# Kernel optimization log

Measured on AMD Instinct MI355X. Metric: run time of the kernel, lower is better.

The kernel has to match this reference:

```python
import jax, jax.numpy as jnp
import numpy as np

DIM = 1024
DIM_HEAD = 64
HEADS = 16
BATCH = 2
SEQ = 2048
SCALE = DIM_HEAD ** -0.5


def setup_inputs() -> dict:
    key = jax.random.key(0)
    ks = jax.random.split(key, 5)
    tokens = jax.random.normal(ks[0], (BATCH, SEQ, DIM), dtype=jnp.float32)
    wq = jax.random.normal(ks[1], (HEADS, DIM, DIM_HEAD), dtype=jnp.float32)
    wk = jax.random.normal(ks[2], (HEADS, DIM, DIM_HEAD), dtype=jnp.float32)
    wv = jax.random.normal(ks[3], (HEADS, DIM, DIM_HEAD), dtype=jnp.float32)
    wo = jax.random.normal(ks[4], (HEADS, DIM_HEAD, DIM), dtype=jnp.float32)
    return {"tokens": tokens, "wq": wq, "wk": wk, "wv": wv, "wo": wo}


def reference(tokens, wq, wk, wv, wo):
    # q, k, v: [b, h, n, dh]
    q = jnp.einsum('bnd,hde->bhne', tokens, wq) * SCALE
    k = jnp.einsum('bnd,hde->bhne', tokens, wk)
    v = jnp.einsum('bnd,hde->bhne', tokens, wv)
    sim = jnp.einsum('bhie,bhje->bhij', q, k)          # [b, h, n, n]
    attn = jax.nn.softmax(sim, axis=-1)
    aggregated = jnp.einsum('bhij,bhje->bhie', attn, v)  # [b, h, n, dh]
    retrieved = jnp.einsum('bhne,hed->bnd', aggregated, wo)  # sum over heads
    return retrieved
```

## Files before the change

kernel.cpp:

```cpp
#include <hip/hip_runtime.h>
#include <hip/hip_fp16.h>
#include <stdint.h>

#define BB 2
#define HH 16
#define SS 2048
#define DD 1024
#define DHH 64
#define QSCALE 0.18033688011112042f

typedef _Float16 half8 __attribute__((ext_vector_type(8)));
typedef _Float16 half4 __attribute__((ext_vector_type(4)));
typedef __fp16 fp16x2 __attribute__((ext_vector_type(2)));
typedef float floatx4 __attribute__((ext_vector_type(4)));

__device__ __forceinline__ floatx4 mfma16(half8 a, half8 b, floatx4 c) {
  return __builtin_amdgcn_mfma_f32_16x16x32_f16(a, b, c, 0, 0, 0);
}
__device__ __forceinline__ floatx4 mfma16k16(half4 a, half4 b, floatx4 c) {
  return __builtin_amdgcn_mfma_f32_16x16x16f16(a, b, c, 0, 0, 0);
}

__device__ __forceinline__ void dma16(const _Float16* g, _Float16* l) {
  __builtin_amdgcn_global_load_lds(
      (const __attribute__((address_space(1))) uint32_t*)g,
      (__attribute__((address_space(3))) uint32_t*)l,
      16, 0, 0);
}

__global__ __launch_bounds__(256) void convert_kernel(
    const float* __restrict__ wq, const float* __restrict__ wk,
    const float* __restrict__ wv, const float* __restrict__ wo,
    _Float16* __restrict__ Wh, _Float16* __restrict__ Wl,
    _Float16* __restrict__ Wot)
{
  __shared__ float St[64][68];
  const int kt = blockIdx.x;
  const int hy = blockIdx.y;
  const int z  = blockIdx.z;
  const int t  = (int)threadIdx.x;
  const int k0 = kt * 64;

  const float* src = (z == 0) ? (wq + hy * (DD * DHH))
                   : (z == 1) ? (wk + hy * (DD * DHH))
                   : (z == 2) ? (wv + hy * (DD * DHH))
                   : wo;

  const int rr = t >> 4, cc = (t & 15) * 4;
  if (z < 3) {
    #pragma unroll
    for (int i = 0; i < 4; ++i)
      *(floatx4*)&St[rr + 16 * i][cc] =
          *(const floatx4*)(src + (k0 + rr + 16 * i) * DHH + cc);
  } else {
    const int d0 = hy * 64;
    #pragma unroll
    for (int i = 0; i < 4; ++i)
      *(floatx4*)&St[rr + 16 * i][cc] =
          *(const floatx4*)(src + (k0 + rr + 16 * i) * 1024 + d0 + cc);
  }
  __syncthreads();

  const int e = t >> 2, kc = (t & 3) * 16;
  if (z < 3) {
    const int n = z * 1024 + hy * 64 + e;
    half8 hi0, hi1, lo0, lo1;
    #pragma unroll
    for (int u = 0; u < 16; ++u) {
      float x = St[kc + u][e];
      _Float16 hh = (_Float16)x;
      _Float16 ll = (_Float16)(x - (float)hh);
      if (u < 8) { hi0[u] = hh; lo0[u] = ll; }
      else       { hi1[u - 8] = hh; lo1[u - 8] = ll; }
    }
    *(half8*)(Wh + n * 1024 + k0 + kc)     = hi0;
    *(half8*)(Wh + n * 1024 + k0 + kc + 8) = hi1;
    *(half8*)(Wl + n * 1024 + k0 + kc)     = lo0;
    *(half8*)(Wl + n * 1024 + k0 + kc + 8) = lo1;
  } else {
    const int d0 = hy * 64;
    half8 hi0, hi1;
    #pragma unroll
    for (int u = 0; u < 16; ++u) {
      _Float16 hh = (_Float16)St[kc + u][e];
      if (u < 8) hi0[u] = hh; else hi1[u - 8] = hh;
    }
    *(half8*)(Wot + (d0 + e) * 1024 + k0 + kc)     = hi0;
    *(half8*)(Wot + (d0 + e) * 1024 + k0 + kc + 8) = hi1;
  }
}

__global__ __launch_bounds__(256) void tokens_split_kernel(
    const float* __restrict__ tokens,
    _Float16* __restrict__ th, _Float16* __restrict__ tl)
{
  const int i = ((int)blockIdx.x * 256 + (int)threadIdx.x) * 8;
  floatx4 x0 = *(const floatx4*)(tokens + i);
  floatx4 x1 = *(const floatx4*)(tokens + i + 4);
  half8 h, l;
  #pragma unroll
  for (int j = 0; j < 8; ++j) {
    float x = (j < 4) ? x0[j] : x1[j - 4];
    _Float16 hh = (_Float16)x;
    h[j] = hh;
    l[j] = (_Float16)(x - (float)hh);
  }
  *(half8*)(th + i) = h;
  *(half8*)(tl + i) = l;
}

__global__ __launch_bounds__(512) void qkv_gemm_kernel(
    const _Float16* __restrict__ th, const _Float16* __restrict__ tl,
    const _Float16* __restrict__ Wh, const _Float16* __restrict__ Wl,
    _Float16* __restrict__ qh, _Float16* __restrict__ ql,
    _Float16* __restrict__ kh, _Float16* __restrict__ kl,
    _Float16* __restrict__ vt)
{
  __shared__ alignas(16) _Float16 sbuf[4][4][128 * 32];

  const int n0 = blockIdx.x * 128;
  const int m0 = blockIdx.y * 128;
  const int zb = n0 >> 10;
  const bool is_v = (zb == 2);
  const int t = (int)threadIdx.x;
  const int lane = t & 63, wid = t >> 6;
  const int l16 = lane & 15, q4 = lane >> 4;
  const int mw = (wid & 3) * 32, nw = (wid >> 2) * 64;

  const int g  = (lane & 7) ^ ((lane >> 3) & 7);
  const int grow  = (lane >> 3) * 2 + (g >> 2);
  const int gcol8 = (g & 3) * 8;
  const int laneoff = (l16 >> 1) * 128 + (((((l16 & 1) << 2) | q4) ^ (l16 >> 1)) * 16);

  const int arr = wid & 3;
  const int rowb = (wid >> 2) * 64;
  const _Float16* src = (arr == 0) ? (th + m0 * 1024)
                      : (arr == 1) ? (Wh + n0 * 1024)
                      : (arr == 2) ? (Wl + n0 * 1024)
                      :              (tl + m0 * 1024);
  const bool stage_active = !(is_v && arr == 3);
  const _Float16* gsrc = src + (rowb + grow) * 1024 + gcol8;

  const floatx4 z4 = {0.0f, 0.0f, 0.0f, 0.0f};
  floatx4 acc[2][4];
  #pragma unroll
  for (int mi = 0; mi < 2; ++mi)
    #pragma unroll
    for (int ni = 0; ni < 4; ++ni) acc[mi][ni] = z4;

  auto stage = [&](int buf, int kt2) {
    if (stage_active) {
      const _Float16* gp = gsrc + kt2 * 32;
      _Float16* dst = &sbuf[buf][arr][rowb * 32];
      #pragma unroll
      for (int j = 0; j < 4; ++j)
        dma16(gp + j * 16 * 1024, dst + j * 16 * 32);
    }
  };

  auto compute = [&](int buf) {
    const char* sAh = (const char*)&sbuf[buf][0][0];
    const char* sBh = (const char*)&sbuf[buf][1][0];
    const char* sBl = (const char*)&sbuf[buf][2][0];
    const char* sAl = (const char*)&sbuf[buf][3][0];
    half8 a_h[2], b_h[4], b_l[4];
    #pragma unroll
    for (int mi = 0; mi < 2; ++mi)
      a_h[mi] = *(const half8*)(sAh + (mw + mi * 16) * 64 + laneoff);
    #pragma unroll
    for (int ni = 0; ni < 4; ++ni) {
      b_h[ni] = *(const half8*)(sBh + (nw + ni * 16) * 64 + laneoff);
      b_l[ni] = *(const half8*)(sBl + (nw + ni * 16) * 64 + laneoff);
    }
    #pragma unroll
    for (int ni = 0; ni < 4; ++ni)
      #pragma unroll
      for (int mi = 0; mi < 2; ++mi)
        acc[mi][ni] = mfma16(a_h[mi], b_h[ni], acc[mi][ni]);
    if (!is_v) {
      half8 a_l[2];
      #pragma unroll
      for (int mi = 0; mi < 2; ++mi)
        a_l[mi] = *(const half8*)(sAl + (mw + mi * 16) * 64 + laneoff);
      #pragma unroll
      for (int ni = 0; ni < 4; ++ni)
        #pragma unroll
        for (int mi = 0; mi < 2; ++mi)
          acc[mi][ni] = mfma16(a_l[mi], b_h[ni], acc[mi][ni]);
    }
    #pragma unroll
    for (int ni = 0; ni < 4; ++ni)
      #pragma unroll
      for (int mi = 0; mi < 2; ++mi)
        acc[mi][ni] = mfma16(a_h[mi], b_l[ni], acc[mi][ni]);
  };

  stage(0, 0);
  stage(1, 1);
  stage(2, 2);

#define QKV_PHASE(P, BUF, VC)                                  \
  asm volatile("s_waitcnt vmcnt(" #VC ")" ::: "memory");       \
  __builtin_amdgcn_s_barrier();                                \
  if ((P) + 3 < 32) stage(((P) + 3) & 3, (P) + 3);             \
  compute(BUF);

  #pragma unroll 1
  for (int p4 = 0; p4 < 28; p4 += 4) {
    QKV_PHASE(p4 + 0, 0, 8)
    QKV_PHASE(p4 + 1, 1, 8)
    QKV_PHASE(p4 + 2, 2, 8)
    QKV_PHASE(p4 + 3, 3, 8)
  }
  QKV_PHASE(28, 0, 8)
  QKV_PHASE(29, 1, 8)
  QKV_PHASE(30, 2, 4)
  QKV_PHASE(31, 3, 0)
#undef QKV_PHASE

  #pragma unroll
  for (int ni = 0; ni < 4; ++ni) {
    const int ncol = n0 + nw + ni * 16;
    const int h = (ncol >> 6) & 15;
    const int e = (ncol & 63) + l16;
    #pragma unroll
    for (int mi = 0; mi < 2; ++mi) {
      #pragma unroll
      for (int r = 0; r < 4; ++r) {
        const int grow2 = m0 + mw + mi * 16 + q4 * 4 + r;
        const int b = grow2 >> 11, s = grow2 & 2047;
        const float v = acc[mi][ni][r];
        const int qkidx = ((b * HH + h) * SS + s) * DHH + e;
        if (zb == 0) {
          const float vs = v * QSCALE;
          const _Float16 hh = (_Float16)vs;
          qh[qkidx] = hh;
          ql[qkidx] = (_Float16)(vs - (float)hh);
        } else if (zb == 1) {
          const _Float16 hh = (_Float16)v;
          kh[qkidx] = hh;
          kl[qkidx] = (_Float16)(v - (float)hh);
        } else {
          const int sl = s & 63;
          const int sp = (s & ~63) | ((sl & 48) >> 2) | ((sl & 12) << 2) | (sl & 3);
          vt[((b * HH + h) * DHH + e) * SS + sp] = (_Float16)v;
        }
      }
    }
  }
}

__global__ __launch_bounds__(512) void attn_kernel(
    const _Float16* __restrict__ qh, const _Float16* __restrict__ ql,
    const _Float16* __restrict__ kh, const _Float16* __restrict__ kl,
    const _Float16* __restrict__ vt, _Float16* __restrict__ agg)
{
  __shared__ _Float16 Kh[2][64][72], Kl[2][64][72];
  __shared__ _Float16 Vs[2][64][64];

  const int qt = blockIdx.x;
  const int h  = blockIdx.y;
  const int b  = blockIdx.z;
  const int bh = b * HH + h;
  const int t = (int)threadIdx.x;
  const int lane = t & 63, wid = t >> 6;
  const int l16 = lane & 15, q4 = lane >> 4;

  const int sr = t >> 3, sc = (t & 7) * 8;
  const int vsw = ((t & 7) ^ (sr & 7)) * 8;

  const int vch0 = ((2 * q4 + 0) ^ (l16 & 7)) * 8;
  const int vch1 = ((2 * q4 + 1) ^ (l16 & 7)) * 8;

  half8 qfh[2], qfl[2];
  {
    const int s = qt * 128 + wid * 16 + l16;
    const int base = (bh * SS + s) * DHH + q4 * 8;
    qfh[0] = *(const half8*)(qh + base);
    qfh[1] = *(const half8*)(qh + base + 32);
    qfl[0] = *(const half8*)(ql + base);
    qfl[1] = *(const half8*)(ql + base + 32);
  }

  const floatx4 z4 = {0.0f, 0.0f, 0.0f, 0.0f};
  floatx4 o[4];
  #pragma unroll
  for (int i = 0; i < 4; ++i) o[i] = z4;
  float m_r = -1e30f;
  float l_lane = 0.0f;

  half8 pK, pL, pV;
  {
    const int gk = (bh * SS + sr) * DHH + sc;
    pK = *(const half8*)(kh + gk);
    pL = *(const half8*)(kl + gk);
    pV = *(const half8*)(vt + (bh * DHH + sr) * SS + sc);
  }
  *(half8*)&Kh[0][sr][sc] = pK;
  *(half8*)&Kl[0][sr][sc] = pL;
  *(half8*)&Vs[0][sr][vsw] = pV;
  __syncthreads();
  {
    const int gk = (bh * SS + 64 + sr) * DHH + sc;
    pK = *(const half8*)(kh + gk);
    pL = *(const half8*)(kl + gk);
    pV = *(const half8*)(vt + (bh * DHH + sr) * SS + 64 + sc);
  }

  auto body = [&](int buf, int kt) {
    floatx4 sv[4];
    __builtin_amdgcn_s_setprio(1);
    #pragma unroll
    for (int sub = 0; sub < 4; ++sub) {
      const half8 ah0 = *(const half8*)&Kh[buf][sub * 16 + l16][q4 * 8];
      const half8 ah1 = *(const half8*)&Kh[buf][sub * 16 + l16][q4 * 8 + 32];
      const half8 al0 = *(const half8*)&Kl[buf][sub * 16 + l16][q4 * 8];
      const half8 al1 = *(const half8*)&Kl[buf][sub * 16 + l16][q4 * 8 + 32];
      floatx4 s4 = z4;
      s4 = mfma16(ah0, qfh[0], s4);
      s4 = mfma16(ah1, qfh[1], s4);
      s4 = mfma16(al0, qfh[0], s4);
      s4 = mfma16(al1, qfh[1], s4);
      s4 = mfma16(ah0, qfl[0], s4);
      s4 = mfma16(ah1, qfl[1], s4);
      sv[sub] = s4;
    }
    __builtin_amdgcn_s_setprio(0);

    float m0 = fmaxf(fmaxf(sv[0][0], sv[0][1]), fmaxf(sv[0][2], sv[0][3]));
    float m1 = fmaxf(fmaxf(sv[1][0], sv[1][1]), fmaxf(sv[1][2], sv[1][3]));
    float m2 = fmaxf(fmaxf(sv[2][0], sv[2][1]), fmaxf(sv[2][2], sv[2][3]));
    float m3 = fmaxf(fmaxf(sv[3][0], sv[3][1]), fmaxf(sv[3][2], sv[3][3]));
    const float mx = fmaxf(fmaxf(m0, m1), fmaxf(m2, m3));

    if (__any(mx > m_r + 8.0f)) {
      float mc = fmaxf(mx, __shfl_xor(mx, 16));
      mc = fmaxf(mc, __shfl_xor(mc, 32));
      const float mnew = fmaxf(m_r, mc);
      const float alpha = exp2f(m_r - mnew);
      m_r = mnew;
      l_lane *= alpha;
      #pragma unroll
      for (int sub = 0; sub < 4; ++sub)
        #pragma unroll
        for (int r = 0; r < 4; ++r) o[sub][r] *= alpha;
    }

    half4 p4[4];
    #pragma unroll
    for (int c = 0; c < 4; ++c) {
      const float p0 = exp2f(sv[c][0] - m_r);
      const float p1 = exp2f(sv[c][1] - m_r);
      const float p2 = exp2f(sv[c][2] - m_r);
      const float p3 = exp2f(sv[c][3] - m_r);
      l_lane += (p0 + p1) + (p2 + p3);
      const fp16x2 a01 = __builtin_amdgcn_cvt_pkrtz(p0, p1);
      const fp16x2 a23 = __builtin_amdgcn_cvt_pkrtz(p2, p3);
      half4 pv;
      pv[0] = (_Float16)a01[0]; pv[1] = (_Float16)a01[1];
      pv[2] = (_Float16)a23[0]; pv[3] = (_Float16)a23[1];
      p4[c] = pv;
    }

    if (kt < 31) {
      *(half8*)&Kh[buf ^ 1][sr][sc] = pK;
      *(half8*)&Kl[buf ^ 1][sr][sc] = pL;
      *(half8*)&Vs[buf ^ 1][sr][vsw] = pV;
    }

    __builtin_amdgcn_s_setprio(1);
    #pragma unroll
    for (int sub = 0; sub < 4; ++sub) {
      const half8 v01 = *(const half8*)&Vs[buf][sub * 16 + l16][vch0];
      const half8 v23 = *(const half8*)&Vs[buf][sub * 16 + l16][vch1];
      const half4 va0 = {v01[0], v01[1], v01[2], v01[3]};
      const half4 va1 = {v01[4], v01[5], v01[6], v01[7]};
      const half4 va2 = {v23[0], v23[1], v23[2], v23[3]};
      const half4 va3 = {v23[4], v23[5], v23[6], v23[7]};
      o[sub] = mfma16k16(va0, p4[0], o[sub]);
      o[sub] = mfma16k16(va1, p4[1], o[sub]);
      o[sub] = mfma16k16(va2, p4[2], o[sub]);
      o[sub] = mfma16k16(va3, p4[3], o[sub]);
    }
    __builtin_amdgcn_s_setprio(0);

    __syncthreads();

    if (kt < 30) {
      const int k2 = (kt + 2) * 64;
      const int gk = (bh * SS + k2 + sr) * DHH + sc;
      pK = *(const half8*)(kh + gk);
      pL = *(const half8*)(kl + gk);
      pV = *(const half8*)(vt + (bh * DHH + sr) * SS + k2 + sc);
    }
  };

  #pragma unroll 1
  for (int kt = 0; kt < 32; kt += 2) {
    body(0, kt);
    body(1, kt + 1);
  }

  float lsum = l_lane;
  lsum += __shfl_xor(lsum, 16);
  lsum += __shfl_xor(lsum, 32);
  const float inv = 1.0f / lsum;
  const int s = qt * 128 + wid * 16 + l16;
  #pragma unroll
  for (int sub = 0; sub < 4; ++sub) {
    half4 ov;
    #pragma unroll
    for (int r = 0; r < 4; ++r) ov[r] = (_Float16)(o[sub][r] * inv);
    *(half4*)(agg + (b * SS + s) * (HH * DHH) + h * DHH + sub * 16 + q4 * 4) = ov;
  }
}

__global__ __launch_bounds__(256) void out_gemm_kernel(
    const _Float16* __restrict__ agg, const _Float16* __restrict__ Wot,
    float* __restrict__ out)
{
  __shared__ alignas(16) _Float16 sbuf[2][2][128 * 32];
  const int n0 = blockIdx.x * 128;
  const int m0 = blockIdx.y * 128;
  const int t = (int)threadIdx.x;
  const int lane = t & 63, wid = t >> 6;
  const int l16 = lane & 15, q4 = lane >> 4;
  const int mw = (wid & 1) * 64, nw = (wid >> 1) * 64;

  const int g  = (lane & 7) ^ ((lane >> 3) & 7);
  const int grow  = (lane >> 3) * 2 + (g >> 2);
  const int gcol8 = (g & 3) * 8;
  const int laneoff = (l16 >> 1) * 128 + (((((l16 & 1) << 2) | q4) ^ (l16 >> 1)) * 16);

  const int arr = wid >> 1;
  const int half64 = (wid & 1) * 64;
  const _Float16* src = (arr == 0) ? (agg + m0 * 1024) : (Wot + n0 * 1024);
  const _Float16* gsrc = src + (half64 + grow) * 1024 + gcol8;

  const floatx4 z4 = {0.0f, 0.0f, 0.0f, 0.0f};
  floatx4 acc[4][4];
  #pragma unroll
  for (int mi = 0; mi < 4; ++mi)
    #pragma unroll
    for (int ni = 0; ni < 4; ++ni) acc[mi][ni] = z4;

  auto stage = [&](int buf, int kt2) {
    const _Float16* gp = gsrc + kt2 * 32;
    _Float16* dst = &sbuf[buf][arr][half64 * 32];
    #pragma unroll
    for (int j = 0; j < 4; ++j)
      dma16(gp + j * 16 * 1024, dst + j * 16 * 32);
  };

  auto compute = [&](int buf) {
    const char* sA = (const char*)&sbuf[buf][0][0];
    const char* sB = (const char*)&sbuf[buf][1][0];
    half8 a_f[4];
    #pragma unroll
    for (int mi = 0; mi < 4; ++mi)
      a_f[mi] = *(const half8*)(sA + (mw + mi * 16) * 64 + laneoff);
    #pragma unroll
    for (int ni = 0; ni < 4; ++ni) {
      const half8 b_f = *(const half8*)(sB + (nw + ni * 16) * 64 + laneoff);
      #pragma unroll
      for (int mi = 0; mi < 4; ++mi)
        acc[mi][ni] = mfma16(a_f[mi], b_f, acc[mi][ni]);
    }
  };

  stage(0, 0);
  __syncthreads();

  #pragma unroll 1
  for (int kt = 0; kt < 32; kt += 2) {
    if (kt + 1 < 32) stage(1, kt + 1);
    compute(0);
    __syncthreads();
    if (kt + 2 < 32) stage(0, kt + 2);
    compute(1);
    __syncthreads();
  }

  #pragma unroll
  for (int ni = 0; ni < 4; ++ni)
    #pragma unroll
    for (int mi = 0; mi < 4; ++mi)
      #pragma unroll
      for (int r = 0; r < 4; ++r)
        out[(m0 + mw + mi * 16 + q4 * 4 + r) * 1024 + n0 + nw + ni * 16 + l16] =
            acc[mi][ni][r];
}

extern "C" void kernel_launch(void* const* d_in, const int* in_sizes, int n_in,
                              void* d_out, int out_size, void* d_ws, size_t ws_size,
                              hipStream_t stream)
{
  const float* tokens = (const float*)d_in[0];
  const float* wq = (const float*)d_in[1];
  const float* wk = (const float*)d_in[2];
  const float* wv = (const float*)d_in[3];
  const float* wo = (const float*)d_in[4];
  float* out = (float*)d_out;

  char* ws = (char*)d_ws;
  _Float16* qh  = (_Float16*)(ws);
  _Float16* ql  = (_Float16*)(ws + 8388608);
  _Float16* kh  = (_Float16*)(ws + 16777216);
  _Float16* kl  = (_Float16*)(ws + 25165824);
  _Float16* vt  = (_Float16*)(ws + 33554432);
  _Float16* Wh  = (_Float16*)(ws + 41943040);
  _Float16* Wl  = (_Float16*)(ws + 48234496);
  _Float16* Wot = (_Float16*)(ws + 54525952);
  _Float16* th  = (_Float16*)(ws + 56623104);
  _Float16* tl  = (_Float16*)(ws + 65011712);
  _Float16* agg = (_Float16*)(ws + 56623104);

  convert_kernel<<<dim3(16, 16, 4), 256, 0, stream>>>(wq, wk, wv, wo, Wh, Wl, Wot);
  tokens_split_kernel<<<2048, 256, 0, stream>>>(tokens, th, tl);
  qkv_gemm_kernel<<<dim3(24, 32), 512, 0, stream>>>(th, tl, Wh, Wl, qh, ql, kh, kl, vt);
  attn_kernel<<<dim3(16, 16, 2), 512, 0, stream>>>(qh, ql, kh, kl, vt, agg);
  out_gemm_kernel<<<dim3(8, 32), 256, 0, stream>>>(agg, Wot, out);
}
```

Before: 287.5 us.

## Load V fragments straight into registers, use fast exp2, deepen out-GEMM pipeline

The attention kernel now loads V tiles directly from global memory into per-lane register fragments, double-buffered across iterations, instead of staging them through shared memory. This removes the LDS store and read traffic for V but adds register pressure. The softmax swaps exp2f for the raw hardware exp2 builtin. The output GEMM moves to 512 threads with a 4-deep shared-memory ring buffer, explicit vmcnt waits and a single barrier per phase, so more async loads are in flight.

Result: slower. 343.9 us (+19.6%).

```diff
diff --git a/kernel.cpp b/kernel.cpp
--- a/kernel.cpp
+++ b/kernel.cpp
@@ -256,7 +256,6 @@
     const _Float16* __restrict__ vt, _Float16* __restrict__ agg)
 {
   __shared__ _Float16 Kh[2][64][72], Kl[2][64][72];
-  __shared__ _Float16 Vs[2][64][64];
 
   const int qt = blockIdx.x;
   const int h  = blockIdx.y;
@@ -267,10 +266,6 @@
   const int l16 = lane & 15, q4 = lane >> 4;
 
   const int sr = t >> 3, sc = (t & 7) * 8;
-  const int vsw = ((t & 7) ^ (sr & 7)) * 8;
-
-  const int vch0 = ((2 * q4 + 0) ^ (l16 & 7)) * 8;
-  const int vch1 = ((2 * q4 + 1) ^ (l16 & 7)) * 8;
 
   half8 qfh[2], qfl[2];
   {
@@ -289,25 +284,35 @@
   float m_r = -1e30f;
   float l_lane = 0.0f;
 
-  half8 pK, pL, pV;
+  const _Float16* vbase = vt + (bh * DHH + l16) * SS + q4 * 16;
+  half8 vfA[8], vfB[8];
+  auto vload = [&](half8* vf, int k0) {
+    #pragma unroll
+    for (int sub = 0; sub < 4; ++sub) {
+      const _Float16* p = vbase + sub * 16 * SS + k0;
+      vf[sub * 2]     = *(const half8*)(p);
+      vf[sub * 2 + 1] = *(const half8*)(p + 8);
+    }
+  };
+
+  half8 pK, pL;
   {
     const int gk = (bh * SS + sr) * DHH + sc;
     pK = *(const half8*)(kh + gk);
     pL = *(const half8*)(kl + gk);
-    pV = *(const half8*)(vt + (bh * DHH + sr) * SS + sc);
-  }
+  }
+  vload(vfA, 0);
   *(half8*)&Kh[0][sr][sc] = pK;
   *(half8*)&Kl[0][sr][sc] = pL;
-  *(half8*)&Vs[0][sr][vsw] = pV;
   __syncthreads();
   {
     const int gk = (bh * SS + 64 + sr) * DHH + sc;
     pK = *(const half8*)(kh + gk);
     pL = *(const half8*)(kl + gk);
-    pV = *(const half8*)(vt + (bh * DHH + sr) * SS + 64 + sc);
-  }
-
-  auto body = [&](int buf, int kt) {
+  }
+  vload(vfB, 64);
+
+  auto body = [&](int buf, int kt, half8 (&vfc)[8]) {
     floatx4 sv[4];
     __builtin_amdgcn_s_setprio(1);
     #pragma unroll
@@ -337,7 +342,7 @@
       float mc = fmaxf(mx, __shfl_xor(mx, 16));
       mc = fmaxf(mc, __shfl_xor(mc, 32));
       const float mnew = fmaxf(m_r, mc);
-      const float alpha = exp2f(m_r - mnew);
+      const float alpha = __builtin_amdgcn_exp2f(m_r - mnew);
       m_r = mnew;
       l_lane *= alpha;
       #pragma unroll
@@ -349,10 +354,10 @@
     half4 p4[4];
     #pragma unroll
     for (int c = 0; c < 4; ++c) {
-      const float p0 = exp2f(sv[c][0] - m_r);
-      const float p1 = exp2f(sv[c][1] - m_r);
-      const float p2 = exp2f(sv[c][2] - m_r);
-      const float p3 = exp2f(sv[c][3] - m_r);
+      const float p0 = __builtin_amdgcn_exp2f(sv[c][0] - m_r);
+      const float p1 = __builtin_amdgcn_exp2f(sv[c][1] - m_r);
+      const float p2 = __builtin_amdgcn_exp2f(sv[c][2] - m_r);
+      const float p3 = __builtin_amdgcn_exp2f(sv[c][3] - m_r);
       l_lane += (p0 + p1) + (p2 + p3);
       const fp16x2 a01 = __builtin_amdgcn_cvt_pkrtz(p0, p1);
       const fp16x2 a23 = __builtin_amdgcn_cvt_pkrtz(p2, p3);
@@ -365,14 +370,13 @@
     if (kt < 31) {
       *(half8*)&Kh[buf ^ 1][sr][sc] = pK;
       *(half8*)&Kl[buf ^ 1][sr][sc] = pL;
-      *(half8*)&Vs[buf ^ 1][sr][vsw] = pV;
     }
 
     __builtin_amdgcn_s_setprio(1);
     #pragma unroll
     for (int sub = 0; sub < 4; ++sub) {
-      const half8 v01 = *(const half8*)&Vs[buf][sub * 16 + l16][vch0];
-      const half8 v23 = *(const half8*)&Vs[buf][sub * 16 + l16][vch1];
+      const half8 v01 = vfc[sub * 2];
+      const half8 v23 = vfc[sub * 2 + 1];
       const half4 va0 = {v01[0], v01[1], v01[2], v01[3]};
       const half4 va1 = {v01[4], v01[5], v01[6], v01[7]};
       const half4 va2 = {v23[0], v23[1], v23[2], v23[3]};
@@ -391,14 +395,14 @@
       const int gk = (bh * SS + k2 + sr) * DHH + sc;
       pK = *(const half8*)(kh + gk);
       pL = *(const half8*)(kl + gk);
-      pV = *(const half8*)(vt + (bh * DHH + sr) * SS + k2 + sc);
+      vload(vfc, k2);
     }
   };
 
   #pragma unroll 1
   for (int kt = 0; kt < 32; kt += 2) {
-    body(0, kt);
-    body(1, kt + 1);
+    body(0, kt, vfA);
+    body(1, kt + 1, vfB);
   }
 
   float lsum = l_lane;
@@ -415,76 +419,86 @@
   }
 }
 
-__global__ __launch_bounds__(256) void out_gemm_kernel(
+__global__ __launch_bounds__(512) void out_gemm_kernel(
     const _Float16* __restrict__ agg, const _Float16* __restrict__ Wot,
     float* __restrict__ out)
 {
-  __shared__ alignas(16) _Float16 sbuf[2][2][128 * 32];
+  __shared__ alignas(16) _Float16 sbuf[4][2][128 * 32];
   const int n0 = blockIdx.x * 128;
   const int m0 = blockIdx.y * 128;
   const int t = (int)threadIdx.x;
   const int lane = t & 63, wid = t >> 6;
   const int l16 = lane & 15, q4 = lane >> 4;
-  const int mw = (wid & 1) * 64, nw = (wid >> 1) * 64;
+  const int mw = (wid & 3) * 32, nw = (wid >> 2) * 64;
 
   const int g  = (lane & 7) ^ ((lane >> 3) & 7);
   const int grow  = (lane >> 3) * 2 + (g >> 2);
   const int gcol8 = (g & 3) * 8;
   const int laneoff = (l16 >> 1) * 128 + (((((l16 & 1) << 2) | q4) ^ (l16 >> 1)) * 16);
 
-  const int arr = wid >> 1;
-  const int half64 = (wid & 1) * 64;
+  const int arr = wid & 1;
+  const int rowq = (wid >> 1) * 32;
   const _Float16* src = (arr == 0) ? (agg + m0 * 1024) : (Wot + n0 * 1024);
-  const _Float16* gsrc = src + (half64 + grow) * 1024 + gcol8;
+  const _Float16* gsrc = src + (rowq + grow) * 1024 + gcol8;
 
   const floatx4 z4 = {0.0f, 0.0f, 0.0f, 0.0f};
-  floatx4 acc[4][4];
-  #pragma unroll
-  for (int mi = 0; mi < 4; ++mi)
+  floatx4 acc[2][4];
+  #pragma unroll
+  for (int mi = 0; mi < 2; ++mi)
     #pragma unroll
     for (int ni = 0; ni < 4; ++ni) acc[mi][ni] = z4;
 
   auto stage = [&](int buf, int kt2) {
     const _Float16* gp = gsrc + kt2 * 32;
-    _Float16* dst = &sbuf[buf][arr][half64 * 32];
-    #pragma unroll
-    for (int j = 0; j < 4; ++j)
+    _Float16* dst = &sbuf[buf][arr][rowq * 32];
+    #pragma unroll
+    for (int j = 0; j < 2; ++j)
       dma16(gp + j * 16 * 1024, dst + j * 16 * 32);
   };
 
   auto compute = [&](int buf) {
     const char* sA = (const char*)&sbuf[buf][0][0];
     const char* sB = (const char*)&sbuf[buf][1][0];
-    half8 a_f[4];
-    #pragma unroll
-    for (int mi = 0; mi < 4; ++mi)
+    half8 a_f[2];
+    #pragma unroll
+    for (int mi = 0; mi < 2; ++mi)
       a_f[mi] = *(const half8*)(sA + (mw + mi * 16) * 64 + laneoff);
     #pragma unroll
     for (int ni = 0; ni < 4; ++ni) {
       const half8 b_f = *(const half8*)(sB + (nw + ni * 16) * 64 + laneoff);
       #pragma unroll
-      for (int mi = 0; mi < 4; ++mi)
+      for (int mi = 0; mi < 2; ++mi)
         acc[mi][ni] = mfma16(a_f[mi], b_f, acc[mi][ni]);
     }
   };
 
   stage(0, 0);
-  __syncthreads();
+  stage(1, 1);
+  stage(2, 2);
+
+#define OUT_PHASE(P, BUF, VC)                                  \
+  asm volatile("s_waitcnt vmcnt(" #VC ")" ::: "memory");       \
+  __builtin_amdgcn_s_barrier();                                \
+  if ((P) + 3 < 32) stage(((P) + 3) & 3, (P) + 3);             \
+  compute(BUF);
 
   #pragma unroll 1
-  for (int kt = 0; kt < 32; kt += 2) {
-    if (kt + 1 < 32) stage(1, kt + 1);
-    compute(0);
-    __syncthreads();
-    if (kt + 2 < 32) stage(0, kt + 2);
-    compute(1);
-    __syncthreads();
-  }
+  for (int p4 = 0; p4 < 28; p4 += 4) {
+    OUT_PHASE(p4 + 0, 0, 4)
+    OUT_PHASE(p4 + 1, 1, 4)
+    OUT_PHASE(p4 + 2, 2, 4)
+    OUT_PHASE(p4 + 3, 3, 4)
+  }
+  OUT_PHASE(28, 0, 4)
+  OUT_PHASE(29, 1, 4)
+  OUT_PHASE(30, 2, 2)
+  OUT_PHASE(31, 3, 0)
+#undef OUT_PHASE
 
   #pragma unroll
   for (int ni = 0; ni < 4; ++ni)
     #pragma unroll
-    for (int mi = 0; mi < 4; ++mi)
+    for (int mi = 0; mi < 2; ++mi)
       #pragma unroll
       for (int r = 0; r < 4; ++r)
         out[(m0 + mw + mi * 16 + q4 * 4 + r) * 1024 + n0 + nw + ni * 16 + l16] =
@@ -519,5 +533,5 @@
   tokens_split_kernel<<<2048, 256, 0, stream>>>(tokens, th, tl);
   qkv_gemm_kernel<<<dim3(24, 32), 512, 0, stream>>>(th, tl, Wh, Wl, qh, ql, kh, kl, vt);
   attn_kernel<<<dim3(16, 16, 2), 512, 0, stream>>>(qh, ql, kh, kl, vt, agg);
-  out_gemm_kernel<<<dim3(8, 32), 256, 0, stream>>>(agg, Wot, out);
-}
+  out_gemm_kernel<<<dim3(8, 32), 512, 0, stream>>>(agg, Wot, out);
+}
```
